# Kernel optimization log

Hardware: AMD Instinct MI355X
Metric: run time of the kernel (lower is better)

Reference implementation:

```python
import jax, jax.numpy as jnp
import numpy as np

N_NODES = 100_000
N_EDGES = 1_600_000
IN_CH = 128
HIDDEN = 48
OUT_CH = 16
NEG_SLOPE = 0.2  # PyG GATConv default LeakyReLU slope


def setup_inputs() -> dict:
    key = jax.random.key(0)
    ks = jax.random.split(key, 8)
    x = jax.random.normal(ks[0], (N_NODES, IN_CH), dtype=jnp.float32)
    edge_index = jax.random.randint(ks[1], (2, N_EDGES), 0, N_NODES, dtype=jnp.int64)
    W = jax.random.normal(ks[2], (IN_CH, HIDDEN), dtype=jnp.float32) / np.sqrt(IN_CH)
    att_src = jax.random.normal(ks[3], (HIDDEN,), dtype=jnp.float32) / np.sqrt(HIDDEN)
    att_dst = jax.random.normal(ks[4], (HIDDEN,), dtype=jnp.float32) / np.sqrt(HIDDEN)
    gat_bias = jax.random.normal(ks[5], (HIDDEN,), dtype=jnp.float32) * 0.01
    lin_W = jax.random.normal(ks[6], (HIDDEN, OUT_CH), dtype=jnp.float32) / np.sqrt(HIDDEN)
    lin_b = jax.random.normal(ks[7], (OUT_CH,), dtype=jnp.float32) * 0.01
    return {"x": x, "edge_index": edge_index, "W": W, "att_src": att_src,
            "att_dst": att_dst, "gat_bias": gat_bias, "lin_W": lin_W, "lin_b": lin_b}


def reference(x, edge_index, W, att_src, att_dst, gat_bias, lin_W, lin_b):
    n = x.shape[0]
    # PyG GATConv adds self loops by default
    loops = jnp.arange(n, dtype=edge_index.dtype)
    src = jnp.concatenate([edge_index[0], loops])  # [E+N] message sources j
    dst = jnp.concatenate([edge_index[1], loops])  # [E+N] message targets i

    h = x @ W                      # [N, H] transformed node features
    a_src = h @ att_src            # [N] per-node source attention term
    a_dst = h @ att_dst            # [N] per-node destination attention term

    logits = jax.nn.leaky_relu(a_src[src] + a_dst[dst], NEG_SLOPE)  # [E+N]
    # segment softmax over incoming edges of each destination node
    m = jax.ops.segment_max(logits, dst, num_segments=n)            # [N]
    e = jnp.exp(logits - m[dst])
    denom = jax.ops.segment_sum(e, dst, num_segments=n)             # [N] (>0: self loop)
    alpha = e / denom[dst]                                          # [E+N]

    agg = jax.ops.segment_sum(h[src] * alpha[:, None], dst, num_segments=n)
    out = jax.nn.elu(agg + gat_bias)          # [N, H]
    # dropout is identity in eval mode
    z = out @ lin_W + lin_b                   # [N, OUT]
    return jax.nn.log_softmax(z, axis=-1)
```

## Files before the change

### kernel.cpp

```cpp
#include <hip/hip_runtime.h>
#include <hip/hip_fp16.h>

#define IN_CH 128
#define HID 48
#define OUT_CH 16
#define NEG_SLOPE 0.2f
#define SCAN_ELEMS 2048
#define ROWB 128
#define WLP 20

__device__ __forceinline__ float leaky(float x) { return x >= 0.f ? x : NEG_SLOPE * x; }
__device__ __forceinline__ float elu(float x) { return x > 0.f ? x : __expf(x) - 1.f; }

__device__ __forceinline__ void load_edge(const void* ei, int E, int is64, int e,
                                          int& s, int& d) {
    if (is64) {
        const long long* p = (const long long*)ei;
        s = (int)p[e];
        d = (int)p[(size_t)E + e];
    } else {
        const int* p = (const int*)ei;
        s = p[e];
        d = p[(size_t)E + e];
    }
}

#define BLK_NODES 256
__global__ __launch_bounds__(256, 2) void k_xw(const float* __restrict__ x,
                                               const float* __restrict__ W,
                                               const float* __restrict__ att_src,
                                               const float* __restrict__ att_dst,
                                               const unsigned* __restrict__ ei,
                                               __half* __restrict__ h2,
                                               float* __restrict__ a_src,
                                               float* __restrict__ a_dst,
                                               int* __restrict__ deg,
                                               int* __restrict__ flag, int N) {
    __shared__ float Wl[IN_CH * HID];
    __shared__ float xl[BLK_NODES * 33];
    const int t = threadIdx.x;
    if (blockIdx.x == 0 && t == 0) {
        unsigned sdet = 0;
        for (int i = 1; i < 128; i += 2) sdet |= ei[i];
        *flag = (sdet == 0) ? 1 : 0;
    }
    for (int i = t; i < IN_CH * HID / 4; i += 256)
        ((float4*)Wl)[i] = ((const float4*)W)[i];
    const int n0 = blockIdx.x * BLK_NODES;
    const int kq = t & 3;
    const int ng = t >> 2;
    const int k0 = kq * 12;

    float acc[4][12];
#pragma unroll
    for (int i = 0; i < 4; ++i)
#pragma unroll
        for (int j = 0; j < 12; ++j) acc[i][j] = 0.f;

    for (int c0 = 0; c0 < IN_CH; c0 += 32) {
        __syncthreads();
#pragma unroll
        for (int p = 0; p < 8; ++p) {
            int id = t + p * 256;
            int row = id >> 3;
            int seg = id & 7;
            int n = n0 + row;
            float4 v = make_float4(0.f, 0.f, 0.f, 0.f);
            if (n < N) v = ((const float4*)(x + (size_t)n * IN_CH + c0))[seg];
            float* dst = &xl[row * 33 + seg * 4];
            dst[0] = v.x; dst[1] = v.y; dst[2] = v.z; dst[3] = v.w;
        }
        __syncthreads();
#pragma unroll 8
        for (int cc = 0; cc < 32; ++cc) {
            int c = c0 + cc;
            float xv[4];
#pragma unroll
            for (int i = 0; i < 4; ++i) xv[i] = xl[(ng * 4 + i) * 33 + cc];
            const float* wr = &Wl[c * HID + k0];
#pragma unroll
            for (int j = 0; j < 12; ++j) {
                float wv = wr[j];
#pragma unroll
                for (int i = 0; i < 4; ++i) acc[i][j] += xv[i] * wv;
            }
        }
    }
#pragma unroll
    for (int i = 0; i < 4; ++i) {
        int n = n0 + ng * 4 + i;
        if (n < N) {
            uint* dst = (uint*)((char*)h2 + (size_t)n * ROWB) + k0 / 2;
#pragma unroll
            for (int j = 0; j < 6; ++j) {
                __half2 hv = __floats2half2_rn(acc[i][2 * j], acc[i][2 * j + 1]);
                dst[j] = *(const uint*)&hv;
            }
        }
    }
#pragma unroll
    for (int p = 0; p < 8; ++p) {
        int id = t + p * 256;
        int row = id >> 3;
        int seg = id & 7;
        int n = n0 + row;
        if (n < N) ((uint*)((char*)h2 + (size_t)n * ROWB))[24 + seg] = 0u;
    }
    float as_[4], ad_[4];
#pragma unroll
    for (int i = 0; i < 4; ++i) {
        float s1 = 0.f, s2 = 0.f;
#pragma unroll
        for (int j = 0; j < 12; ++j) {
            float a = acc[i][j];
            s1 += a * att_src[k0 + j];
            s2 += a * att_dst[k0 + j];
        }
        s1 += __shfl_xor(s1, 1); s1 += __shfl_xor(s1, 2);
        s2 += __shfl_xor(s2, 1); s2 += __shfl_xor(s2, 2);
        as_[i] = s1; ad_[i] = s2;
    }
    if (kq == 0) {
#pragma unroll
        for (int i = 0; i < 4; ++i) {
            int n = n0 + ng * 4 + i;
            if (n < N) { a_src[n] = as_[i]; a_dst[n] = ad_[i]; }
        }
    }
    {
        int n = n0 + t;
        if (n < N) deg[n] = 0;
    }
}

__global__ __launch_bounds__(256) void k_count(const void* __restrict__ ei,
                                               const int* __restrict__ flag,
                                               int* __restrict__ deg,
                                               unsigned short* __restrict__ rank, int E) {
    int e = blockIdx.x * blockDim.x + threadIdx.x;
    if (e >= E) return;
    int d = (*flag) ? (int)((const long long*)ei)[(size_t)E + e]
                    : ((const int*)ei)[(size_t)E + e];
    rank[e] = (unsigned short)atomicAdd(&deg[d], 1);
}

__global__ __launch_bounds__(256) void k_scan_block(const int* __restrict__ deg,
                                                    int* __restrict__ rowptr,
                                                    int* __restrict__ bsum, int N) {
    __shared__ int sm[256];
    const int t = threadIdx.x;
    const int base = blockIdx.x * SCAN_ELEMS + t * 8;
    int v[8];
    int s = 0;
#pragma unroll
    for (int i = 0; i < 8; ++i) {
        v[i] = (base + i < N) ? deg[base + i] : 0;
        s += v[i];
    }
    sm[t] = s;
    __syncthreads();
    for (int off = 1; off < 256; off <<= 1) {
        int y = (t >= off) ? sm[t - off] : 0;
        __syncthreads();
        sm[t] += y;
        __syncthreads();
    }
    int run = sm[t] - s;
#pragma unroll
    for (int i = 0; i < 8; ++i) {
        if (base + i < N) rowptr[base + i] = run;
        run += v[i];
    }
    if (t == 255) bsum[blockIdx.x] = sm[255];
}

__global__ __launch_bounds__(256) void k_scan_add(int* __restrict__ rowptr,
                                                  const int* __restrict__ bsum, int N, int E) {
    __shared__ int soff;
    const int chunk = (int)(((long long)blockIdx.x * 256) / SCAN_ELEMS);
    if (threadIdx.x == 0) {
        int run = 0;
        for (int b = 0; b < chunk; ++b) run += bsum[b];
        soff = run;
    }
    __syncthreads();
    int i = blockIdx.x * 256 + threadIdx.x;
    if (i == 0) rowptr[N] = E;
    if (i >= N) return;
    rowptr[i] += soff;
}

__global__ __launch_bounds__(256) void k_scatter(const void* __restrict__ ei,
                                                 const int* __restrict__ flag,
                                                 const int* __restrict__ rowptr,
                                                 const unsigned short* __restrict__ rank,
                                                 unsigned* __restrict__ srcs, int E) {
    int e = blockIdx.x * blockDim.x + threadIdx.x;
    if (e >= E) return;
    int is64 = *flag;
    int s, d;
    load_edge(ei, E, is64, e, s, d);
    int pos = rowptr[d] + (int)rank[e];
    srcs[pos] = (unsigned)s;
}

__global__ __launch_bounds__(256) void k_gat_node(const int* __restrict__ rowptr,
                                                  const unsigned* __restrict__ srcs,
                                                  const float* __restrict__ a_src,
                                                  const float* __restrict__ a_dst,
                                                  const __half* __restrict__ h2,
                                                  const float* __restrict__ gat_bias,
                                                  const float* __restrict__ lin_W,
                                                  const float* __restrict__ lin_b,
                                                  float* __restrict__ out, int N) {
    __shared__ float Wl[HID * WLP];
    __shared__ float lb[OUT_CH];
    __shared__ float gb[HID];
    __shared__ float o_sm[4][HID];
    __shared__ unsigned long long evb[4][64];
    const int t = threadIdx.x;
    for (int i = t; i < HID * OUT_CH; i += 256) Wl[(i >> 4) * WLP + (i & 15)] = lin_W[i];
    if (t < OUT_CH) lb[t] = lin_b[t];
    if (t >= 64 && t < 64 + HID) gb[t - 64] = gat_bias[t - 64];
    __syncthreads();

    const int wv = t >> 6;
    const int lane = t & 63;
    const int slot = lane >> 4;
    const int c = lane & 15;
    const int n = blockIdx.x * 4 + wv;
    const bool active = n < N;

    if (active) {
        const int base = rowptr[n];
        const int deg = rowptr[n + 1] - base;
        const float adn = a_dst[n];
        const float ev_self = __expf(fminf(leaky(a_src[n] + adn), 50.f));
        const char* hb = (const char*)h2;

        float a0 = 0.f, a1 = 0.f, a2 = 0.f, a3 = 0.f;
        float evsum = (lane == 0) ? ev_self : 0.f;
        if (slot == 0) {
            uint2 hv = *(const uint2*)(hb + (size_t)n * ROWB + 8 * c);
            __half2 h01 = *(const __half2*)&hv.x;
            __half2 h23 = *(const __half2*)&hv.y;
            a0 = ev_self * __low2float(h01);
            a1 = ev_self * __high2float(h01);
            a2 = ev_self * __low2float(h23);
            a3 = ev_self * __high2float(h23);
        }
        for (int c0 = 0; c0 < deg; c0 += 64) {
            int j = c0 + lane;
            unsigned s = 0;
            float ev = 0.f;
            if (j < deg) {
                s = srcs[base + j];
                ev = __expf(fminf(leaky(a_src[s] + adn), 50.f));
            }
            evsum += ev;
            evb[wv][lane] = ((unsigned long long)__float_as_uint(ev) << 32) | s;
            const int cnt = (deg - c0 < 64) ? (deg - c0) : 64;
#pragma unroll 4
            for (int jj = slot; jj < cnt; jj += 4) {
                unsigned long long pr = evb[wv][jj];
                unsigned sj = (unsigned)pr;
                float evj = __uint_as_float((unsigned)(pr >> 32));
                uint2 hv = *(const uint2*)(hb + (size_t)sj * ROWB + 8 * c);
                __half2 h01 = *(const __half2*)&hv.x;
                __half2 h23 = *(const __half2*)&hv.y;
                a0 += evj * __low2float(h01);
                a1 += evj * __high2float(h01);
                a2 += evj * __low2float(h23);
                a3 += evj * __high2float(h23);
            }
        }
#pragma unroll
        for (int off = 1; off < 64; off <<= 1) evsum += __shfl_xor(evsum, off);
        a0 += __shfl_xor(a0, 16); a0 += __shfl_xor(a0, 32);
        a1 += __shfl_xor(a1, 16); a1 += __shfl_xor(a1, 32);
        a2 += __shfl_xor(a2, 16); a2 += __shfl_xor(a2, 32);
        a3 += __shfl_xor(a3, 16); a3 += __shfl_xor(a3, 32);
        const float inv = 1.f / evsum;
        if (slot == 0 && c < 12) {
            float4 v = make_float4(elu(a0 * inv + gb[4 * c + 0]),
                                   elu(a1 * inv + gb[4 * c + 1]),
                                   elu(a2 * inv + gb[4 * c + 2]),
                                   elu(a3 * inv + gb[4 * c + 3]));
            *(float4*)&o_sm[wv][4 * c] = v;
        }
    }
    __syncthreads();

    if (active) {
        const float* o = o_sm[wv];
        float z = 0.f;
#pragma unroll
        for (int i = 0; i < 12; ++i) {
            int k = 12 * slot + i;
            z += o[k] * Wl[k * WLP + c];
        }
        z += __shfl_xor(z, 16); z += __shfl_xor(z, 32);
        z += lb[c];
        float mx = z;
#pragma unroll
        for (int off = 8; off; off >>= 1) mx = fmaxf(mx, __shfl_xor(mx, off, 16));
        float ev = __expf(z - mx);
#pragma unroll
        for (int off = 8; off; off >>= 1) ev += __shfl_xor(ev, off, 16);
        float lse = mx + __logf(ev);
        if (slot == 0) out[(size_t)n * OUT_CH + c] = z - lse;
    }
}

extern "C" void kernel_launch(void* const* d_in, const int* in_sizes, int n_in,
                              void* d_out, int out_size, void* d_ws, size_t ws_size,
                              hipStream_t stream) {
    const float* x = (const float*)d_in[0];
    const void* edge_index = d_in[1];
    const float* W = (const float*)d_in[2];
    const float* att_src = (const float*)d_in[3];
    const float* att_dst = (const float*)d_in[4];
    const float* gat_bias = (const float*)d_in[5];
    const float* lin_W = (const float*)d_in[6];
    const float* lin_b = (const float*)d_in[7];
    float* out = (float*)d_out;

    const int N = in_sizes[0] / IN_CH;
    const int E = in_sizes[1] / 2;

    __half* h2 = (__half*)d_ws;
    float* a_src = (float*)((char*)d_ws + (size_t)N * ROWB);
    float* a_dst = a_src + N;
    int* rowptr = (int*)(a_dst + N);
    int* degbuf = rowptr + N + 1;
    int* bsum = degbuf + N;
    int* flag = bsum + 64;
    unsigned short* rank = (unsigned short*)(flag + 1);
    unsigned* srcs =
        (unsigned*)(((uintptr_t)(rank + E) + 3) & ~(uintptr_t)3);

    const int nodeBlocks = (N + 255) / 256;
    const int edgeBlocks = (E + 255) / 256;
    const int scanBlocks = (N + SCAN_ELEMS - 1) / SCAN_ELEMS;

    k_xw<<<(N + BLK_NODES - 1) / BLK_NODES, 256, 0, stream>>>(
        x, W, att_src, att_dst, (const unsigned*)edge_index,
        h2, a_src, a_dst, degbuf, flag, N);
    k_count<<<edgeBlocks, 256, 0, stream>>>(edge_index, flag, degbuf, rank, E);
    k_scan_block<<<scanBlocks, 256, 0, stream>>>(degbuf, rowptr, bsum, N);
    k_scan_add<<<nodeBlocks, 256, 0, stream>>>(rowptr, bsum, N, E);
    k_scatter<<<edgeBlocks, 256, 0, stream>>>(edge_index, flag, rowptr, rank, srcs, E);
    k_gat_node<<<(N + 3) / 4, 256, 0, stream>>>(rowptr, srcs, a_src, a_dst,
                                                h2, gat_bias, lin_W, lin_b, out, N);
}
```

Before: 208.2 us.

## Fuse degree counting into XW kernel and software-pipeline gather loads

Degree zeroing and the int64/int32 flag detection move into a new small init kernel. The edge-degree atomic counting is folded into the tail of the dense XW kernel, with each block handling a contiguous chunk of edges, so the separate count launch disappears and the atomics can overlap with the matmul work. In the aggregation kernel, the inner gather loop is software-pipelined: the next neighbor's half-precision row is loaded before the current one is accumulated, to hide memory latency. The cost is an extra tiny launch, more register pressure in k_xw (which has launch bounds of 2 blocks), and less parallelism for the atomics, since only about 391 blocks now cover 1.6M edges.

```diff
diff --git a/kernel.cpp b/kernel.cpp
--- a/kernel.cpp
+++ b/kernel.cpp
@@ -25,25 +25,34 @@
     }
 }
 
+__global__ __launch_bounds__(256) void k_init(const unsigned* __restrict__ ei,
+                                              int* __restrict__ deg,
+                                              int* __restrict__ flag, int N) {
+    int i = blockIdx.x * blockDim.x + threadIdx.x;
+    if (i < N) deg[i] = 0;
+    if (i == 0) {
+        unsigned sdet = 0;
+        for (int k = 1; k < 128; k += 2) sdet |= ei[k];
+        *flag = (sdet == 0) ? 1 : 0;
+    }
+}
+
 #define BLK_NODES 256
 __global__ __launch_bounds__(256, 2) void k_xw(const float* __restrict__ x,
                                                const float* __restrict__ W,
                                                const float* __restrict__ att_src,
                                                const float* __restrict__ att_dst,
-                                               const unsigned* __restrict__ ei,
+                                               const void* __restrict__ ei,
                                                __half* __restrict__ h2,
                                                float* __restrict__ a_src,
                                                float* __restrict__ a_dst,
                                                int* __restrict__ deg,
-                                               int* __restrict__ flag, int N) {
+                                               const int* __restrict__ flag,
+                                               unsigned short* __restrict__ rank,
+                                               int N, int E) {
     __shared__ float Wl[IN_CH * HID];
     __shared__ float xl[BLK_NODES * 33];
     const int t = threadIdx.x;
-    if (blockIdx.x == 0 && t == 0) {
-        unsigned sdet = 0;
-        for (int i = 1; i < 128; i += 2) sdet |= ei[i];
-        *flag = (sdet == 0) ? 1 : 0;
-    }
     for (int i = t; i < IN_CH * HID / 4; i += 256)
         ((float4*)Wl)[i] = ((const float4*)W)[i];
     const int n0 = blockIdx.x * BLK_NODES;
@@ -128,20 +137,17 @@
         }
     }
     {
-        int n = n0 + t;
-        if (n < N) deg[n] = 0;
-    }
-}
-
-__global__ __launch_bounds__(256) void k_count(const void* __restrict__ ei,
-                                               const int* __restrict__ flag,
-                                               int* __restrict__ deg,
-                                               unsigned short* __restrict__ rank, int E) {
-    int e = blockIdx.x * blockDim.x + threadIdx.x;
-    if (e >= E) return;
-    int d = (*flag) ? (int)((const long long*)ei)[(size_t)E + e]
-                    : ((const int*)ei)[(size_t)E + e];
-    rank[e] = (unsigned short)atomicAdd(&deg[d], 1);
+        const int nb = gridDim.x;
+        const int per = (E + nb - 1) / nb;
+        const int e0 = blockIdx.x * per;
+        const int e1 = (e0 + per < E) ? e0 + per : E;
+        const int is64 = *flag;
+        for (int e = e0 + t; e < e1; e += 256) {
+            int d = is64 ? (int)((const long long*)ei)[(size_t)E + e]
+                         : ((const int*)ei)[(size_t)E + e];
+            rank[e] = (unsigned short)atomicAdd(&deg[d], 1);
+        }
+    }
 }
 
 __global__ __launch_bounds__(256) void k_scan_block(const int* __restrict__ deg,
@@ -260,14 +266,30 @@
             evsum += ev;
             evb[wv][lane] = ((unsigned long long)__float_as_uint(ev) << 32) | s;
             const int cnt = (deg - c0 < 64) ? (deg - c0) : 64;
-#pragma unroll 4
-            for (int jj = slot; jj < cnt; jj += 4) {
-                unsigned long long pr = evb[wv][jj];
-                unsigned sj = (unsigned)pr;
-                float evj = __uint_as_float((unsigned)(pr >> 32));
-                uint2 hv = *(const uint2*)(hb + (size_t)sj * ROWB + 8 * c);
-                __half2 h01 = *(const __half2*)&hv.x;
-                __half2 h23 = *(const __half2*)&hv.y;
+            int jj = slot;
+            unsigned long long prA = 0;
+            uint2 hvA = make_uint2(0u, 0u);
+            if (jj < cnt) {
+                prA = evb[wv][jj];
+                hvA = *(const uint2*)(hb + (size_t)(unsigned)prA * ROWB + 8 * c);
+            }
+#pragma unroll 2
+            for (; jj + 4 < cnt; jj += 4) {
+                unsigned long long prB = evb[wv][jj + 4];
+                uint2 hvB = *(const uint2*)(hb + (size_t)(unsigned)prB * ROWB + 8 * c);
+                float evj = __uint_as_float((unsigned)(prA >> 32));
+                __half2 h01 = *(const __half2*)&hvA.x;
+                __half2 h23 = *(const __half2*)&hvA.y;
+                a0 += evj * __low2float(h01);
+                a1 += evj * __high2float(h01);
+                a2 += evj * __low2float(h23);
+                a3 += evj * __high2float(h23);
+                prA = prB; hvA = hvB;
+            }
+            if (jj < cnt) {
+                float evj = __uint_as_float((unsigned)(prA >> 32));
+                __half2 h01 = *(const __half2*)&hvA.x;
+                __half2 h23 = *(const __half2*)&hvA.y;
                 a0 += evj * __low2float(h01);
                 a1 += evj * __high2float(h01);
                 a2 += evj * __low2float(h23);
@@ -343,10 +365,9 @@
     const int edgeBlocks = (E + 255) / 256;
     const int scanBlocks = (N + SCAN_ELEMS - 1) / SCAN_ELEMS;
 
+    k_init<<<nodeBlocks, 256, 0, stream>>>((const unsigned*)edge_index, degbuf, flag, N);
     k_xw<<<(N + BLK_NODES - 1) / BLK_NODES, 256, 0, stream>>>(
-        x, W, att_src, att_dst, (const unsigned*)edge_index,
-        h2, a_src, a_dst, degbuf, flag, N);
-    k_count<<<edgeBlocks, 256, 0, stream>>>(edge_index, flag, degbuf, rank, E);
+        x, W, att_src, att_dst, edge_index, h2, a_src, a_dst, degbuf, flag, rank, N, E);
     k_scan_block<<<scanBlocks, 256, 0, stream>>>(degbuf, rowptr, bsum, N);
     k_scan_add<<<nodeBlocks, 256, 0, stream>>>(rowptr, bsum, N, E);
     k_scatter<<<edgeBlocks, 256, 0, stream>>>(edge_index, flag, rowptr, rank, srcs, E);
```

New measurement: 206.9 us. Within noise of the previous version (-0.6%).
